# Kernel tuning notes

Hardware: AMD Instinct MI355X
Metric: run time of the kernel (lower is better)

## Reference

```python
import jax, jax.numpy as jnp
import numpy as np

N_NODES = 100000
N_EDGES = 3200000
HID = 128
NUM_ATTR = 10000
K = 3
EPS = 1e-5


def setup_inputs() -> dict:
    key = jax.random.key(0)
    ks = jax.random.split(key, 8)
    x_idx = jax.random.randint(ks[0], (N_NODES,), 0, NUM_ATTR)
    edge_index = jax.random.randint(ks[1], (2, N_EDGES), 0, N_NODES)
    edge_weight = jax.random.uniform(ks[2], (N_EDGES,), dtype=jnp.float32)
    emb = jax.random.normal(ks[3], (NUM_ATTR, HID), dtype=jnp.float32) * 0.1
    Wt = jax.random.normal(ks[4], (K, HID, HID), dtype=jnp.float32) * (1.0 / np.sqrt(HID))
    bt = jnp.zeros((K, HID), jnp.float32)
    Wc = jax.random.normal(ks[5], (K, 2 * HID, HID), dtype=jnp.float32) * (1.0 / np.sqrt(2 * HID))
    bc = jnp.zeros((K, HID), jnp.float32)
    cg_gamma = jnp.ones((K, HID), jnp.float32)
    cg_beta = jnp.zeros((K, HID), jnp.float32)
    cg_alpha = jnp.ones((K, HID), jnp.float32)
    gn_gamma = jnp.ones((K - 1, HID), jnp.float32)
    gn_beta = jnp.zeros((K - 1, HID), jnp.float32)
    gn_alpha = jnp.ones((K - 1, HID), jnp.float32)
    return dict(x_idx=x_idx, edge_index=edge_index, edge_weight=edge_weight, emb=emb,
                Wt=Wt, bt=bt, Wc=Wc, bc=bc, cg_gamma=cg_gamma, cg_beta=cg_beta,
                cg_alpha=cg_alpha, gn_gamma=gn_gamma, gn_beta=gn_beta, gn_alpha=gn_alpha)


def graph_norm(x, gamma, beta, alpha):
    # GraphNorm over node dim: out = gamma*(x - alpha*mean)/sqrt(var+eps) + beta
    mean = jnp.mean(x, axis=0, keepdims=True)
    sub = x - alpha * mean
    var = jnp.mean(sub * sub, axis=0, keepdims=True)
    return gamma * sub * jax.lax.rsqrt(var + EPS) + beta


def build_mean_adj_weights(edge_index, edge_weight, n_nodes):
    # aggr='mean': w_e = edge_weight_e / deg[row_e], deg from row sums (deg<0.5 -> +1)
    row = edge_index[0]
    deg = jax.ops.segment_sum(edge_weight, row, num_segments=n_nodes)
    deg = jnp.where(deg < 0.5, deg + 1.0, deg)
    inv_deg = 1.0 / deg
    return edge_weight * inv_deg[row]


def conv_layer(x_, row, col, w, Wt, bt, Wc, bc, g, b, a):
    h = jax.nn.relu(x_ @ Wt + bt)                                   # [N, HID]
    m = jax.ops.segment_sum(w[:, None] * h[col], row, num_segments=x_.shape[0])  # adj @ h
    m = graph_norm(m, g, b, a)
    return jnp.concatenate([m, x_], axis=-1) @ Wc + bc


def reference(x_idx, edge_index, edge_weight, emb, Wt, bt, Wc, bc,
              cg_gamma, cg_beta, cg_alpha, gn_gamma, gn_beta, gn_alpha):
    row, col = edge_index[0], edge_index[1]
    w = build_mean_adj_weights(edge_index, edge_weight, x_idx.shape[0])
    x = emb[x_idx]  # embedding lookup; dropout p=0 -> identity
    for i in range(K - 1):
        x = conv_layer(x, row, col, w, Wt[i], bt[i], Wc[i], bc[i],
                       cg_gamma[i], cg_beta[i], cg_alpha[i])
        x = graph_norm(x, gn_gamma[i], gn_beta[i], gn_alpha[i])
        x = jax.nn.relu(x)
    x = conv_layer(x, row, col, w, Wt[K - 1], bt[K - 1], Wc[K - 1], bc[K - 1],
                   cg_gamma[K - 1], cg_beta[K - 1], cg_alpha[K - 1])
    return x
```

## Files before the change

kernel.cpp:

```cpp
#include <hip/hip_runtime.h>
#include <cstdio>


#define HID 128

typedef __attribute__((ext_vector_type(8))) short short8;
typedef __attribute__((ext_vector_type(4))) float floatx4;

__device__ __forceinline__ unsigned short f2bf(float f) {
    unsigned u = __float_as_uint(f);
    unsigned r = (u + 0x7FFFu + ((u >> 16) & 1u)) >> 16;
    return (unsigned short)r;
}
__device__ __forceinline__ float bflo(unsigned u) { return __uint_as_float(u << 16); }
__device__ __forceinline__ float bfhi(unsigned u) { return __uint_as_float(u & 0xFFFF0000u); }

#define NB 512
#define RPB 196
#define CAPB 8192
#define TILE_A 2048

__global__ __launch_bounds__(256) void k_binA(
    const int* __restrict__ row, const int* __restrict__ col,
    const float* __restrict__ ew, int2* __restrict__ binned,
    unsigned* __restrict__ cursor, int E) {
    __shared__ int2 stag[TILE_A];
    __shared__ unsigned short bof[TILE_A];
    __shared__ unsigned hist[NB], scanned[NB], bump[NB];
    __shared__ int delta[NB];
    __shared__ unsigned scanw[256];
    int t = threadIdx.x;
    int tileBase = blockIdx.x * TILE_A;
    int tcnt = min(TILE_A, E - tileBase);

    hist[t] = 0; hist[t + 256] = 0;
    __syncthreads();

    int myb[8]; int2 myv[8];
#pragma unroll
    for (int i = 0; i < 8; ++i) {
        int idx = t + i * 256;
        if (idx < tcnt) {
            int e = tileBase + idx;
            int r = row[e];
            int c = col[e];
            float w = ew[e];
            int b = r / RPB;
            int rl = r - b * RPB;
            myb[i] = b;
            myv[i] = make_int2((rl << 17) | c, __float_as_int(w));
            atomicAdd(&hist[b], 1u);
        } else {
            myb[i] = -1;
            myv[i] = make_int2(0, 0);
        }
    }
    __syncthreads();

    unsigned h0 = hist[2 * t], h1 = hist[2 * t + 1];
    unsigned p = h0 + h1;
    scanw[t] = p;
    __syncthreads();
    for (int o = 1; o < 256; o <<= 1) {
        unsigned x = (t >= o) ? scanw[t - o] : 0u;
        __syncthreads();
        scanw[t] += x;
        __syncthreads();
    }
    unsigned excl = scanw[t] - p;
    scanned[2 * t] = excl;          bump[2 * t] = excl;
    scanned[2 * t + 1] = excl + h0; bump[2 * t + 1] = excl + h0;
    __syncthreads();

#pragma unroll
    for (int j = 0; j < 2; ++j) {
        int b = t + j * 256;
        unsigned c = hist[b];
        if (c) {
            unsigned old = atomicAdd(&cursor[b], c);
            delta[b] = (int)((unsigned)b * CAPB + old) - (int)scanned[b];
        }
    }
    __syncthreads();

#pragma unroll
    for (int i = 0; i < 8; ++i) {
        if (myb[i] >= 0) {
            unsigned s = atomicAdd(&bump[myb[i]], 1u);
            stag[s] = myv[i];
            bof[s] = (unsigned short)myb[i];
        }
    }
    __syncthreads();

    for (int i = t; i < tcnt; i += 256) {
        int b = bof[i];
        int dst = delta[b] + i;
        if (dst < (b + 1) * CAPB) binned[dst] = stag[i];
    }
}

__global__ void k_bscan(const unsigned* __restrict__ cursor, unsigned* __restrict__ outbase) {
    __shared__ unsigned scanw[256];
    int t = threadIdx.x;
    unsigned h0 = min(cursor[2 * t], (unsigned)CAPB);
    unsigned h1 = min(cursor[2 * t + 1], (unsigned)CAPB);
    unsigned p = h0 + h1;
    scanw[t] = p;
    __syncthreads();
    for (int o = 1; o < 256; o <<= 1) {
        unsigned x = (t >= o) ? scanw[t - o] : 0u;
        __syncthreads();
        scanw[t] += x;
        __syncthreads();
    }
    unsigned excl = scanw[t] - p;
    outbase[2 * t] = excl;
    outbase[2 * t + 1] = excl + h0;
}

__global__ __launch_bounds__(256) void k_binB(
    const int2* __restrict__ binned, const unsigned* __restrict__ cursor,
    const unsigned* __restrict__ outbase, int2* __restrict__ edge_s,
    unsigned* __restrict__ endp, unsigned* __restrict__ cntg, int N) {
    __shared__ unsigned hist[256], bump[256], scanw[256];
    __shared__ float wsum[256], inv[256];
    int b = blockIdx.x, t = threadIdx.x;
    size_t base_in = (size_t)b * CAPB;
    unsigned cntb = min(cursor[b], (unsigned)CAPB);
    unsigned outb = outbase[b];

    hist[t] = 0;
    wsum[t] = 0.f;
    __syncthreads();
    for (unsigned i = t; i < cntb; i += 256) {
        int2 v = binned[base_in + i];
        unsigned rl = ((unsigned)v.x) >> 17;
        atomicAdd(&hist[rl], 1u);
        atomicAdd(&wsum[rl], __int_as_float(v.y));
    }
    __syncthreads();

    unsigned h = hist[t];
    scanw[t] = h;
    __syncthreads();
    for (int o = 1; o < 256; o <<= 1) {
        unsigned x = (t >= o) ? scanw[t - o] : 0u;
        __syncthreads();
        scanw[t] += x;
        __syncthreads();
    }
    unsigned excl = scanw[t] - h;
    bump[t] = excl;
    float d = wsum[t];
    d = (d < 0.5f) ? d + 1.0f : d;
    inv[t] = 1.0f / d;
    int grow = b * RPB + t;
    if (t < RPB && grow < N) {
        endp[grow] = outb + excl + h;
        cntg[grow] = h;
    }
    __syncthreads();

    for (unsigned i = t; i < cntb; i += 256) {
        int2 v = binned[base_in + i];
        unsigned rl = ((unsigned)v.x) >> 17;
        unsigned pos = outb + atomicAdd(&bump[rl], 1u);
        float w = __int_as_float(v.y) * inv[rl];
        edge_s[pos] = make_int2(v.x & 0x1FFFF, __float_as_int(w));
    }
}

__global__ void k_prepw(const float* __restrict__ Wt, const float* __restrict__ Wc,
                        unsigned short* __restrict__ WtT, unsigned short* __restrict__ WcT) {
    int tid = blockIdx.x * blockDim.x + threadIdx.x;
    const int T1 = 3 * 128 * 128;
    const int T2 = 3 * 256 * 128;
    if (tid < T1) {
        int l = tid >> 14, rem = tid & 16383;
        int n = rem >> 7, k = rem & 127;
        WtT[tid] = f2bf(Wt[l * 16384 + k * 128 + n]);
    } else if (tid < T1 + T2) {
        int t2 = tid - T1;
        int l = t2 >> 15, rem = t2 & 32767;
        int n = rem >> 8, k = rem & 255;
        WcT[t2] = f2bf(Wc[l * 32768 + k * 128 + n]);
    }
}

#define GM_ROWS 128
#define LDSP 136

__global__ __launch_bounds__(256) void k_gemm(
    const float* __restrict__ X1, const int* __restrict__ G1,
    const float* __restrict__ AB1, int relu1,
    const float* __restrict__ X2, const int* __restrict__ G2,
    const float* __restrict__ AB2, int relu2,
    const unsigned short* __restrict__ Wn, int Kpitch, int nstage,
    const float* __restrict__ bias, void* __restrict__ Y, int relu_out, int out_bf16,
    float* __restrict__ Sout, int N) {
    __shared__ unsigned short Ws[128 * LDSP];
    __shared__ unsigned short Xs[128 * LDSP];
    __shared__ float sred[4][256];
    int t = threadIdx.x;
    int rowBase = blockIdx.x * GM_ROWS;
    int lane = t & 63, wave = t >> 6;
    int quad = lane >> 4, l16 = lane & 15;

    floatx4 acc[2][8];
#pragma unroll
    for (int i = 0; i < 2; ++i)
#pragma unroll
        for (int j = 0; j < 8; ++j) acc[i][j] = (floatx4){0.f, 0.f, 0.f, 0.f};

    int kg = (t & 15) * 8;
    int r0 = t >> 4;

    for (int s = 0; s < nstage; ++s) {
        const float* Xp = s ? X2 : X1;
        const int* Gp = s ? G2 : G1;
        const float* ABp = s ? AB2 : AB1;
        int rl = s ? relu2 : relu1;
        int koff = s * 128;

#pragma unroll
        for (int j = 0; j < 8; ++j) {
            int n = r0 + 16 * j;
            *(short8*)&Ws[n * LDSP + kg] =
                *(const short8*)&Wn[(size_t)n * Kpitch + koff + kg];
        }
        floatx4 Av0 = {1.f, 1.f, 1.f, 1.f}, Av1 = Av0;
        floatx4 Bv0 = {0.f, 0.f, 0.f, 0.f}, Bv1 = Bv0;
        if (ABp) {
            Av0 = *(const floatx4*)&ABp[kg];
            Av1 = *(const floatx4*)&ABp[kg + 4];
            Bv0 = *(const floatx4*)&ABp[HID + kg];
            Bv1 = *(const floatx4*)&ABp[HID + kg + 4];
        }
#pragma unroll
        for (int j = 0; j < 8; ++j) {
            int r = r0 + 16 * j;
            int grow = rowBase + r;
            floatx4 x0 = {0.f, 0.f, 0.f, 0.f}, x1 = x0;
            if (grow < N) {
                size_t srow = Gp ? (size_t)Gp[grow] : (size_t)grow;
                x0 = *(const floatx4*)&Xp[srow * HID + kg];
                x1 = *(const floatx4*)&Xp[srow * HID + kg + 4];
            }
            if (ABp) {
#pragma unroll
                for (int c = 0; c < 4; ++c) {
                    x0[c] = fmaf(x0[c], Av0[c], Bv0[c]);
                    x1[c] = fmaf(x1[c], Av1[c], Bv1[c]);
                }
                if (rl) {
#pragma unroll
                    for (int c = 0; c < 4; ++c) {
                        x0[c] = fmaxf(x0[c], 0.f);
                        x1[c] = fmaxf(x1[c], 0.f);
                    }
                }
            }
            short8 st;
            st[0] = (short)f2bf(x0[0]); st[1] = (short)f2bf(x0[1]);
            st[2] = (short)f2bf(x0[2]); st[3] = (short)f2bf(x0[3]);
            st[4] = (short)f2bf(x1[0]); st[5] = (short)f2bf(x1[1]);
            st[6] = (short)f2bf(x1[2]); st[7] = (short)f2bf(x1[3]);
            *(short8*)&Xs[r * LDSP + kg] = st;
        }
        __syncthreads();

#pragma unroll
        for (int ks = 0; ks < 4; ++ks) {
            int kb = ks * 32 + quad * 8;
            short8 a0 = *(const short8*)&Xs[(wave * 32 + l16) * LDSP + kb];
            short8 a1 = *(const short8*)&Xs[(wave * 32 + 16 + l16) * LDSP + kb];
#pragma unroll
            for (int ni = 0; ni < 8; ++ni) {
                short8 b = *(const short8*)&Ws[(ni * 16 + l16) * LDSP + kb];
                acc[0][ni] = __builtin_amdgcn_mfma_f32_16x16x32_bf16(a0, b, acc[0][ni], 0, 0, 0);
                acc[1][ni] = __builtin_amdgcn_mfma_f32_16x16x32_bf16(a1, b, acc[1][ni], 0, 0, 0);
            }
        }
        __syncthreads();
    }

    float s1[8], s2[8];
#pragma unroll
    for (int ni = 0; ni < 8; ++ni) { s1[ni] = 0.f; s2[ni] = 0.f; }

#pragma unroll
    for (int mi = 0; mi < 2; ++mi) {
#pragma unroll
        for (int ni = 0; ni < 8; ++ni) {
            int gcol = ni * 16 + l16;
            float bv = bias[gcol];
#pragma unroll
            for (int reg = 0; reg < 4; ++reg) {
                int grow = rowBase + wave * 32 + mi * 16 + quad * 4 + reg;
                if (grow < N) {
                    float v = acc[mi][ni][reg] + bv;
                    if (relu_out) v = fmaxf(v, 0.f);
                    s1[ni] += v;
                    s2[ni] += v * v;
                    if (out_bf16)
                        ((unsigned short*)Y)[(size_t)grow * HID + gcol] = f2bf(v);
                    else
                        ((float*)Y)[(size_t)grow * HID + gcol] = v;
                }
            }
        }
    }

    if (Sout) {
#pragma unroll
        for (int ni = 0; ni < 8; ++ni) {
            s1[ni] += __shfl_xor(s1[ni], 16);
            s1[ni] += __shfl_xor(s1[ni], 32);
            s2[ni] += __shfl_xor(s2[ni], 16);
            s2[ni] += __shfl_xor(s2[ni], 32);
        }
        if (lane < 16) {
#pragma unroll
            for (int ni = 0; ni < 8; ++ni) {
                sred[wave][ni * 16 + l16] = s1[ni];
                sred[wave][128 + ni * 16 + l16] = s2[ni];
            }
        }
        __syncthreads();
        float v = sred[0][t & 255];
        if (t < 256) {
            v = sred[0][t] + sred[1][t] + sred[2][t] + sred[3][t];
            atomicAdd(&Sout[(blockIdx.x & 15) * 256 + t], v);
        }
    }
}

#define AGG_R 4

__global__ __launch_bounds__(256) void k_agg(
    const unsigned short* __restrict__ H, const int2* __restrict__ es,
    const unsigned* __restrict__ endp, const unsigned* __restrict__ cnt,
    float* __restrict__ M, float* __restrict__ Spart, int N) {
    __shared__ float sb[4][256];
    int t = threadIdx.x;
    int wv = t >> 6, lane = t & 63;
    int fo = lane * 2;
    int rowBase = blockIdx.x * (4 * AGG_R) + wv * AGG_R;
    float s1a = 0.f, s1b = 0.f, s2a = 0.f, s2b = 0.f;

    for (int j = 0; j < AGG_R; ++j) {
        int rowi = rowBase + j;
        if (rowi >= N) break;
        unsigned e = endp[rowi];
        unsigned p = e - cnt[rowi];
        float a0 = 0.f, a1 = 0.f;
        for (; p + 7 < e; p += 8) {
            int2 ee[8];
            unsigned hh[8];
#pragma unroll
            for (int q = 0; q < 8; ++q) ee[q] = es[p + q];
#pragma unroll
            for (int q = 0; q < 8; ++q)
                hh[q] = *(const unsigned*)&H[(size_t)ee[q].x * HID + fo];
#pragma unroll
            for (int q = 0; q < 8; ++q) {
                float w = __int_as_float(ee[q].y);
                a0 = fmaf(w, bflo(hh[q]), a0);
                a1 = fmaf(w, bfhi(hh[q]), a1);
            }
        }
        for (; p < e; ++p) {
            int2 e0 = es[p];
            unsigned h0 = *(const unsigned*)&H[(size_t)e0.x * HID + fo];
            float w0 = __int_as_float(e0.y);
            a0 = fmaf(w0, bflo(h0), a0);
            a1 = fmaf(w0, bfhi(h0), a1);
        }
        s1a += a0; s1b += a1;
        s2a += a0 * a0; s2b += a1 * a1;
        *(float2*)&M[(size_t)rowi * HID + fo] = make_float2(a0, a1);
    }

    sb[wv][fo] = s1a;
    sb[wv][fo + 1] = s1b;
    sb[wv][128 + fo] = s2a;
    sb[wv][128 + fo + 1] = s2b;
    __syncthreads();
    {
        float v = sb[0][t] + sb[1][t] + sb[2][t] + sb[3][t];
        atomicAdd(&Spart[(blockIdx.x & 15) * 256 + t], v);
    }
}

__global__ void k_finalize(const float* __restrict__ S, const float* __restrict__ gamma,
                           const float* __restrict__ beta, const float* __restrict__ alpha,
                           float* __restrict__ AB, float invN) {
    int f = threadIdx.x;
    float sum = 0.f, sq = 0.f;
#pragma unroll
    for (int c = 0; c < 16; ++c) {
        sum += S[c * 256 + f];
        sq += S[c * 256 + 128 + f];
    }
    float mu = sum * invN;
    float ex2 = sq * invN;
    float a = alpha[f];
    float var = ex2 - 2.f * a * mu * mu + a * a * mu * mu;
    float rs = rsqrtf(var + 1e-5f);
    float A = gamma[f] * rs;
    float B = beta[f] - A * a * mu;
    AB[f] = A;
    AB[HID + f] = B;
}

extern "C" void kernel_launch(void* const* d_in, const int* in_sizes, int n_in,
                              void* d_out, int out_size, void* d_ws, size_t ws_size,
                              hipStream_t stream) {
    const int*   x_idx = (const int*)d_in[0];
    const int*   ei    = (const int*)d_in[1];
    const float* ew    = (const float*)d_in[2];
    const float* emb   = (const float*)d_in[3];
    const float* Wt    = (const float*)d_in[4];
    const float* bt    = (const float*)d_in[5];
    const float* Wc    = (const float*)d_in[6];
    const float* bc    = (const float*)d_in[7];
    const float* cg_g  = (const float*)d_in[8];
    const float* cg_b  = (const float*)d_in[9];
    const float* cg_a  = (const float*)d_in[10];
    const float* gn_g  = (const float*)d_in[11];
    const float* gn_b  = (const float*)d_in[12];
    const float* gn_a  = (const float*)d_in[13];
    const int N = in_sizes[0];
    const int E = in_sizes[2];
    const int* row = ei;
    const int* col = ei + E;

    char* ws = (char*)d_ws;
    size_t off = 0;
    auto alloc = [&](size_t bytes) -> void* {
        size_t o = (off + 511) & ~(size_t)511;
        off = o + bytes;
        return (void*)(ws + o);
    };
    const int SSTRIDE = 16 * 256;
    unsigned* cursor = (unsigned*)alloc(NB * 4);
    float*    Spart  = (float*)alloc(5 * SSTRIDE * 4);
    size_t zero_end = off;
    unsigned* outbase = (unsigned*)alloc(NB * 4);
    unsigned* endp    = (unsigned*)alloc((size_t)N * 4);
    unsigned* cnt     = (unsigned*)alloc((size_t)N * 4);
    float*    AB      = (float*)alloc(5 * 256 * 4);
    unsigned short* WtT = (unsigned short*)alloc((size_t)3 * 128 * 128 * 2);
    unsigned short* WcT = (unsigned short*)alloc((size_t)3 * 128 * 256 * 2);
    int2*     binned  = (int2*)alloc((size_t)NB * CAPB * 8);
    int2*     edge_s  = (int2*)alloc((size_t)E * 8);
    unsigned short* H = (unsigned short*)alloc((size_t)N * HID * 2);
    float*    X       = (float*)alloc((size_t)N * HID * 4);
    float*    M       = (float*)alloc((size_t)N * HID * 4);
    if (off > ws_size) {
        fprintf(stderr, "kernel_launch: ws too small (%zu > %zu)\n", off, ws_size);
        return;
    }

    hipMemsetAsync(d_ws, 0, zero_end, stream);

    k_prepw<<<(3 * 128 * 128 + 3 * 256 * 128 + 255) / 256, 256, 0, stream>>>(Wt, Wc, WtT, WcT);
    k_binA<<<(E + TILE_A - 1) / TILE_A, 256, 0, stream>>>(row, col, ew, binned, cursor, E);
    k_bscan<<<1, 256, 0, stream>>>(cursor, outbase);
    k_binB<<<NB, 256, 0, stream>>>(binned, cursor, outbase, edge_s, endp, cnt, N);

    int gemm_blocks = (N + GM_ROWS - 1) / GM_ROWS;
    auto gemm = [&](const float* X1, const int* G1, const float* AB1, int rl1,
                    const float* X2, const int* G2, const float* AB2, int rl2,
                    const unsigned short* Wn, int Kpitch, int nstage,
                    const float* bias, void* Y, int relu_out, int out_bf16,
                    float* Sout) {
        k_gemm<<<gemm_blocks, 256, 0, stream>>>(X1, G1, AB1, rl1, X2, G2, AB2, rl2,
                                                Wn, Kpitch, nstage, bias, Y,
                                                relu_out, out_bf16, Sout, N);
    };
    int aggB = (N + 4 * AGG_R - 1) / (4 * AGG_R);
    auto agg = [&](int stage) {
        k_agg<<<aggB, 256, 0, stream>>>(H, edge_s, endp, cnt, M,
                                        Spart + stage * SSTRIDE, N);
    };
    auto fin = [&](int stage, const float* g, const float* b, const float* a) {
        k_finalize<<<1, 128, 0, stream>>>(Spart + stage * SSTRIDE, g, b, a,
                                          AB + stage * 256, 1.0f / (float)N);
    };

    gemm(emb, x_idx, nullptr, 0, nullptr, nullptr, nullptr, 0, WtT, 128, 1, bt,
         H, 1, 1, nullptr);
    agg(0);
    fin(0, cg_g, cg_b, cg_a);
    gemm(M, nullptr, AB + 0 * 256, 0, emb, x_idx, nullptr, 0, WcT, 256, 2, bc,
         X, 0, 0, Spart + 1 * SSTRIDE);
    fin(1, gn_g, gn_b, gn_a);

    gemm(X, nullptr, AB + 1 * 256, 1, nullptr, nullptr, nullptr, 0,
         WtT + 16384, 128, 1, bt + 128, H, 1, 1, nullptr);
    agg(2);
    fin(2, cg_g + 128, cg_b + 128, cg_a + 128);
    gemm(M, nullptr, AB + 2 * 256, 0, X, nullptr, AB + 1 * 256, 1,
         WcT + 32768, 256, 2, bc + 128, X, 0, 0, Spart + 3 * SSTRIDE);
    fin(3, gn_g + 128, gn_b + 128, gn_a + 128);

    gemm(X, nullptr, AB + 3 * 256, 1, nullptr, nullptr, nullptr, 0,
         WtT + 2 * 16384, 128, 1, bt + 256, H, 1, 1, nullptr);
    agg(4);
    fin(4, cg_g + 256, cg_b + 256, cg_a + 256);
    gemm(M, nullptr, AB + 4 * 256, 0, X, nullptr, AB + 3 * 256, 1,
         WcT + 2 * 32768, 256, 2, bc + 256, d_out, 0, 0, nullptr);
}
```

Before: 859.9 us.

## Gather 16-byte feature chunks per lane with four edges per wave in aggregation

The aggregation kernel now splits each wave into four 16-lane groups. Each group handles a different edge, and each lane loads a uint4 (8 bf16 features) instead of a single 32-bit pair. Partial sums are combined across groups with xor shuffles, and each lane then writes out its two assigned features. This cuts the number of gather load instructions and raises memory-level parallelism per edge row, at the cost of extra shuffle reductions and a padded tail loop that loads a dummy row with zero weight.

```diff
diff --git a/kernel.cpp b/kernel.cpp
--- a/kernel.cpp
+++ b/kernel.cpp
@@ -345,8 +345,11 @@
     __shared__ float sb[4][256];
     int t = threadIdx.x;
     int wv = t >> 6, lane = t & 63;
-    int fo = lane * 2;
+    int grp = lane >> 4;
+    int l16 = lane & 15;
+    const uint4* __restrict__ H4 = (const uint4*)H;
     int rowBase = blockIdx.x * (4 * AGG_R) + wv * AGG_R;
+    int fo = l16 * 8 + grp * 2;
     float s1a = 0.f, s1b = 0.f, s2a = 0.f, s2b = 0.f;
 
     for (int j = 0; j < AGG_R; ++j) {
@@ -354,32 +357,61 @@
         if (rowi >= N) break;
         unsigned e = endp[rowi];
         unsigned p = e - cnt[rowi];
-        float a0 = 0.f, a1 = 0.f;
-        for (; p + 7 < e; p += 8) {
-            int2 ee[8];
-            unsigned hh[8];
-#pragma unroll
-            for (int q = 0; q < 8; ++q) ee[q] = es[p + q];
-#pragma unroll
-            for (int q = 0; q < 8; ++q)
-                hh[q] = *(const unsigned*)&H[(size_t)ee[q].x * HID + fo];
-#pragma unroll
-            for (int q = 0; q < 8; ++q) {
+
+        float acc[8];
+#pragma unroll
+        for (int i = 0; i < 8; ++i) acc[i] = 0.f;
+
+        for (; p + 15 < e; p += 16) {
+            int2 ee[4];
+#pragma unroll
+            for (int q = 0; q < 4; ++q) ee[q] = es[p + 4 * q + grp];
+            uint4 hh[4];
+#pragma unroll
+            for (int q = 0; q < 4; ++q)
+                hh[q] = H4[(size_t)ee[q].x * 16 + l16];
+            __builtin_amdgcn_sched_barrier(0);
+#pragma unroll
+            for (int q = 0; q < 4; ++q) {
                 float w = __int_as_float(ee[q].y);
-                a0 = fmaf(w, bflo(hh[q]), a0);
-                a1 = fmaf(w, bfhi(hh[q]), a1);
+                acc[0] = fmaf(w, bflo(hh[q].x), acc[0]);
+                acc[1] = fmaf(w, bfhi(hh[q].x), acc[1]);
+                acc[2] = fmaf(w, bflo(hh[q].y), acc[2]);
+                acc[3] = fmaf(w, bfhi(hh[q].y), acc[3]);
+                acc[4] = fmaf(w, bflo(hh[q].z), acc[4]);
+                acc[5] = fmaf(w, bfhi(hh[q].z), acc[5]);
+                acc[6] = fmaf(w, bflo(hh[q].w), acc[6]);
+                acc[7] = fmaf(w, bfhi(hh[q].w), acc[7]);
             }
         }
-        for (; p < e; ++p) {
-            int2 e0 = es[p];
-            unsigned h0 = *(const unsigned*)&H[(size_t)e0.x * HID + fo];
-            float w0 = __int_as_float(e0.y);
-            a0 = fmaf(w0, bflo(h0), a0);
-            a1 = fmaf(w0, bfhi(h0), a1);
-        }
-        s1a += a0; s1b += a1;
-        s2a += a0 * a0; s2b += a1 * a1;
-        *(float2*)&M[(size_t)rowi * HID + fo] = make_float2(a0, a1);
+        for (; p < e; p += 4) {
+            unsigned idx = p + grp;
+            int2 e0 = make_int2(0, 0);
+            if (idx < e) e0 = es[idx];
+            uint4 h = H4[(size_t)e0.x * 16 + l16];
+            float w = __int_as_float(e0.y);
+            acc[0] = fmaf(w, bflo(h.x), acc[0]);
+            acc[1] = fmaf(w, bfhi(h.x), acc[1]);
+            acc[2] = fmaf(w, bflo(h.y), acc[2]);
+            acc[3] = fmaf(w, bfhi(h.y), acc[3]);
+            acc[4] = fmaf(w, bflo(h.z), acc[4]);
+            acc[5] = fmaf(w, bfhi(h.z), acc[5]);
+            acc[6] = fmaf(w, bflo(h.w), acc[6]);
+            acc[7] = fmaf(w, bfhi(h.w), acc[7]);
+        }
+
+#pragma unroll
+        for (int i = 0; i < 8; ++i) {
+            acc[i] += __shfl_xor(acc[i], 16);
+            acc[i] += __shfl_xor(acc[i], 32);
+        }
+        float va = (grp & 2) ? ((grp & 1) ? acc[6] : acc[4])
+                             : ((grp & 1) ? acc[2] : acc[0]);
+        float vb = (grp & 2) ? ((grp & 1) ? acc[7] : acc[5])
+                             : ((grp & 1) ? acc[3] : acc[1]);
+        *(float2*)&M[(size_t)rowi * HID + fo] = make_float2(va, vb);
+        s1a += va; s1b += vb;
+        s2a += va * va; s2b += vb * vb;
     }
 
     sb[wv][fo] = s1a;
```

Measured after the change: 780.4 us. 9.3% less time.
